# Performance work log

Hardware: AMD Instinct MI355X
Metric: run time of the kernel (lower is better)

The kernel has to match this reference:

```python
import jax, jax.numpy as jnp
import numpy as np

B, L, H = 8, 4096, 1024
S = 32            # sentences (sep tokens) per sample, fixed for stackability
SEP_ID = 102      # BERT [SEP]
NUM_LABELS = 2
LN_EPS = 1e-5


def _make_ids_and_mask():
    rng = np.random.default_rng(0)
    ids = rng.integers(1000, 30000, size=(B, L))
    for i in range(B):
        pos = np.sort(rng.choice(np.arange(1, L), size=S, replace=False))
        ids[i, pos] = SEP_ID
    mask = np.ones((B, L), dtype=np.int32)
    return jnp.asarray(ids, dtype=jnp.int64), jnp.asarray(mask)


def setup_inputs() -> dict:
    key = jax.random.key(0)
    ks = jax.random.split(key, 4)
    input_ids, attention_mask = _make_ids_and_mask()
    std = 0.02
    return {
        "seq": jax.random.normal(ks[0], (B, L, H), dtype=jnp.float32),
        "input_ids": input_ids,
        "attention_mask": attention_mask,
        "W1": jax.random.normal(ks[1], (H, H), dtype=jnp.float32) * std,
        "b1": jnp.zeros((H,), jnp.float32),
        "ln_g": jnp.ones((H,), jnp.float32),
        "ln_b": jnp.zeros((H,), jnp.float32),
        "W2": jax.random.normal(ks[2], (H, NUM_LABELS), dtype=jnp.float32) * std,
        "b2": jnp.zeros((NUM_LABELS,), jnp.float32),
    }


def _segment_means(seq, input_ids, attention_mask):
    # sep positions per sample, fixed count S -> [B, S]
    sep_pos = jax.vmap(
        lambda ids: jnp.nonzero(ids == SEP_ID, size=S, fill_value=L - 1)[0]
    )(input_ids)
    bounds = jnp.concatenate(
        [jnp.zeros((seq.shape[0], 1), sep_pos.dtype), sep_pos], axis=1
    )  # [B, S+1]
    st, ed = bounds[:, :-1], bounds[:, 1:]  # inclusive span [st, ed]

    m = attention_mask.astype(seq.dtype)[..., None]            # [B,L,1]
    # exclusive prefix sums -> sum over [st, ed] = P[ed+1] - P[st]
    P = jnp.pad(jnp.cumsum(seq * m, axis=1), ((0, 0), (1, 0), (0, 0)))   # [B,L+1,H]
    C = jnp.pad(jnp.cumsum(attention_mask.astype(jnp.int32), axis=1), ((0, 0), (1, 0)))

    sums = (jnp.take_along_axis(P, (ed + 1)[..., None], axis=1)
            - jnp.take_along_axis(P, st[..., None], axis=1))   # [B,S,H]
    cnts = (jnp.take_along_axis(C, ed + 1, axis=1)
            - jnp.take_along_axis(C, st, axis=1))              # [B,S]
    cnts = jnp.maximum(cnts, 1).astype(seq.dtype)
    return sums / cnts[..., None]


def reference(seq, input_ids, attention_mask, W1, b1, ln_g, ln_b, W2, b2):
    reps = _segment_means(seq, input_ids, attention_mask)      # [B,S,H]
    h = jnp.einsum("bsh,hk->bsk", reps, W1) + b1
    mu = jnp.mean(h, axis=-1, keepdims=True)
    var = jnp.var(h, axis=-1, keepdims=True)
    h = (h - mu) * jax.lax.rsqrt(var + LN_EPS) * ln_g + ln_b
    h = jax.nn.gelu(h, approximate=False)   # torch nn.GELU default (erf); dropout is eval-mode identity
    return jnp.einsum("bsk,kn->bsn", h, W2) + b2               # [B,S,num_labels]
```

## Files before the change

### kernel.cpp

```cpp
#include <hip/hip_runtime.h>
#include <math.h>

#define BB 8
#define LL 4096
#define HH 1024
#define SS 32
#define SEPID 102
#define NROWS 256
#define TOK 64

__global__ __launch_bounds__(256) void prep_kernel(
    const int* __restrict__ ids, const int* __restrict__ mask,
    float* __restrict__ cnts, unsigned char* __restrict__ segcode) {
  int b = blockIdx.x;
  int tid = threadIdx.x;
  __shared__ int spos_raw[SS];
  __shared__ int spos[SS];
  __shared__ int scnt[SS];
  __shared__ int nsep;
  if (tid == 0) nsep = 0;
  if (tid < SS) { scnt[tid] = 0; spos_raw[tid] = LL - 1; }
  __syncthreads();
  const int* idb = ids + (size_t)b * LL;
  const int* mb  = mask + (size_t)b * LL;
  for (int t = tid; t < LL; t += blockDim.x) {
    if (idb[t] == SEPID) {
      int slot = atomicAdd(&nsep, 1);
      if (slot < SS) spos_raw[slot] = t;
    }
  }
  __syncthreads();
  if (tid < SS) {
    int p = spos_raw[tid];
    int rank = 0;
    for (int j = 0; j < SS; j++) {
      int q = spos_raw[j];
      rank += (q < p) || (q == p && j < tid);
    }
    spos[rank] = p;
  }
  __syncthreads();
  for (int t = tid; t < LL; t += blockDim.x) {
    int r = 0;
#pragma unroll
    for (int j = 0; j < SS; j++) r += (spos[j] < t) ? 1 : 0;
    int issep = (idb[t] == SEPID) ? 1 : 0;
    segcode[(size_t)b * LL + t] = (unsigned char)((r << 1) | issep);
    if (mb[t]) {
      if (issep) {
        atomicAdd(&scnt[r], 1);
        if (r + 1 < SS) atomicAdd(&scnt[r + 1], 1);
      } else if (r < SS) {
        atomicAdd(&scnt[r], 1);
      }
    }
  }
  __syncthreads();
  if (tid < SS) cnts[b * SS + tid] = (float)max(scnt[tid], 1);
}

__device__ __forceinline__ void flush_seg(float* __restrict__ sums, int b,
                                          int seg, int tid, const float4& acc) {
  if (seg >= 0) {
    float* p = sums + ((size_t)(b * SS + seg)) * HH + tid * 4;
    atomicAdd(p + 0, acc.x);
    atomicAdd(p + 1, acc.y);
    atomicAdd(p + 2, acc.z);
    atomicAdd(p + 3, acc.w);
  }
}

__global__ __launch_bounds__(256) void segsum_kernel(
    const float4* __restrict__ seq, const int* __restrict__ mask,
    const unsigned char* __restrict__ segcode, float* __restrict__ sums) {
  const int chunks = LL / TOK;
  int b = blockIdx.x / chunks;
  int c = blockIdx.x % chunks;
  int t0 = c * TOK;
  int tid = threadIdx.x;
  __shared__ int scode[TOK];
  if (tid < TOK) {
    int t = t0 + tid;
    int cd = segcode[(size_t)b * LL + t];
    int m = mask[(size_t)b * LL + t];
    int r = cd >> 1, issep = cd & 1;
    int live = (issep || r < SS) ? 1 : 0;
    scode[tid] = cd | ((m && live) ? 0x100 : 0);
  }
  __syncthreads();
  float4 acc = make_float4(0.f, 0.f, 0.f, 0.f);
  int curseg = -1;
  const float4* rowbase = seq + (size_t)(b * LL + t0) * (HH / 4) + tid;
  for (int i = 0; i < TOK; i++) {
    float4 v = rowbase[(size_t)i * (HH / 4)];
    int cd = scode[i];
    int r = (cd >> 1) & 0x3F;
    int issep = cd & 1;
    float mf = (cd & 0x100) ? 1.f : 0.f;
    v.x *= mf; v.y *= mf; v.z *= mf; v.w *= mf;
    if (issep) {
      if (curseg != r) {
        flush_seg(sums, b, curseg, tid, acc);
        acc = make_float4(0.f, 0.f, 0.f, 0.f);
      }
      acc.x += v.x; acc.y += v.y; acc.z += v.z; acc.w += v.w;
      flush_seg(sums, b, r, tid, acc);
      if (r + 1 < SS) { curseg = r + 1; acc = v; }
      else { curseg = -1; acc = make_float4(0.f, 0.f, 0.f, 0.f); }
    } else {
      int sg = (r < SS) ? r : -1;
      if (sg != curseg) {
        flush_seg(sums, b, curseg, tid, acc);
        curseg = sg;
        acc = make_float4(0.f, 0.f, 0.f, 0.f);
      }
      acc.x += v.x; acc.y += v.y; acc.z += v.z; acc.w += v.w;
    }
  }
  flush_seg(sums, b, curseg, tid, acc);
}

__global__ __launch_bounds__(256) void gemm1_kernel(
    const float* __restrict__ sums, const float* __restrict__ cnts,
    const float* __restrict__ W1, const float* __restrict__ b1,
    float* __restrict__ h1) {
  __shared__ float As[32][33];
  __shared__ float Bs[32][33];
  __shared__ float inv[32];
  int bj = blockIdx.x;
  int bi = blockIdx.y;
  int tid = threadIdx.x;
  int r0 = bi * 32, c0 = bj * 32;
  if (tid < 32) inv[tid] = 1.0f / cnts[r0 + tid];
  __syncthreads();
  int tx = tid & 15, ty = tid >> 4;
  int la_k = tid & 31;
  int la_i = tid >> 5;
  float acc00 = 0.f, acc01 = 0.f, acc10 = 0.f, acc11 = 0.f;
  for (int k0 = 0; k0 < HH; k0 += 32) {
#pragma unroll
    for (int p = 0; p < 4; p++) {
      int i = la_i + p * 8;
      As[i][la_k] = sums[(size_t)(r0 + i) * HH + k0 + la_k] * inv[i];
      Bs[i][la_k] = W1[(size_t)(k0 + i) * HH + c0 + la_k];
    }
    __syncthreads();
#pragma unroll
    for (int kk = 0; kk < 32; kk++) {
      float a0 = As[ty * 2][kk];
      float a1 = As[ty * 2 + 1][kk];
      float b0 = Bs[kk][tx * 2];
      float b1v = Bs[kk][tx * 2 + 1];
      acc00 += a0 * b0; acc01 += a0 * b1v;
      acc10 += a1 * b0; acc11 += a1 * b1v;
    }
    __syncthreads();
  }
  int r = r0 + ty * 2, cc = c0 + tx * 2;
  h1[(size_t)r * HH + cc]           = acc00 + b1[cc];
  h1[(size_t)r * HH + cc + 1]       = acc01 + b1[cc + 1];
  h1[(size_t)(r + 1) * HH + cc]     = acc10 + b1[cc];
  h1[(size_t)(r + 1) * HH + cc + 1] = acc11 + b1[cc + 1];
}

__global__ __launch_bounds__(256) void final_kernel(
    const float* __restrict__ h1, const float* __restrict__ ln_g,
    const float* __restrict__ ln_b, const float* __restrict__ W2,
    const float* __restrict__ b2, float* __restrict__ out) {
  int r = blockIdx.x;
  int tid = threadIdx.x;
  const float4* x4 = (const float4*)(h1 + (size_t)r * HH);
  float4 x = x4[tid];
  float s = x.x + x.y + x.z + x.w;
  float sq = x.x * x.x + x.y * x.y + x.z * x.z + x.w * x.w;
  __shared__ float redA[4], redB[4];
#pragma unroll
  for (int off = 32; off >= 1; off >>= 1) {
    s += __shfl_down(s, off, 64);
    sq += __shfl_down(sq, off, 64);
  }
  int wave = tid >> 6, lane = tid & 63;
  if (lane == 0) { redA[wave] = s; redB[wave] = sq; }
  __syncthreads();
  float ts = redA[0] + redA[1] + redA[2] + redA[3];
  float tq = redB[0] + redB[1] + redB[2] + redB[3];
  float mean = ts * (1.0f / HH);
  float var = tq * (1.0f / HH) - mean * mean;
  float rinv = rsqrtf(var + 1e-5f);
  float4 g4 = ((const float4*)ln_g)[tid];
  float4 bb4 = ((const float4*)ln_b)[tid];
  float xs[4] = {x.x, x.y, x.z, x.w};
  float gs[4] = {g4.x, g4.y, g4.z, g4.w};
  float bs[4] = {bb4.x, bb4.y, bb4.z, bb4.w};
  float o0 = 0.f, o1 = 0.f;
  int h = tid * 4;
#pragma unroll
  for (int j = 0; j < 4; j++) {
    float y = (xs[j] - mean) * rinv * gs[j] + bs[j];
    float gel = 0.5f * y * (1.0f + erff(y * 0.70710678118654752440f));
    o0 += gel * W2[(size_t)(h + j) * 2 + 0];
    o1 += gel * W2[(size_t)(h + j) * 2 + 1];
  }
#pragma unroll
  for (int off = 32; off >= 1; off >>= 1) {
    o0 += __shfl_down(o0, off, 64);
    o1 += __shfl_down(o1, off, 64);
  }
  __syncthreads();
  if (lane == 0) { redA[wave] = o0; redB[wave] = o1; }
  __syncthreads();
  if (tid == 0) {
    float r0 = redA[0] + redA[1] + redA[2] + redA[3] + b2[0];
    float r1 = redB[0] + redB[1] + redB[2] + redB[3] + b2[1];
    out[(size_t)r * 2 + 0] = r0;
    out[(size_t)r * 2 + 1] = r1;
  }
}

extern "C" void kernel_launch(void* const* d_in, const int* in_sizes, int n_in,
                              void* d_out, int out_size, void* d_ws, size_t ws_size,
                              hipStream_t stream) {
  (void)in_sizes; (void)n_in; (void)out_size; (void)ws_size;
  const float* seq  = (const float*)d_in[0];
  const int*   ids  = (const int*)d_in[1];
  const int*   mask = (const int*)d_in[2];
  const float* W1   = (const float*)d_in[3];
  const float* b1   = (const float*)d_in[4];
  const float* ln_g = (const float*)d_in[5];
  const float* ln_b = (const float*)d_in[6];
  const float* W2   = (const float*)d_in[7];
  const float* b2   = (const float*)d_in[8];
  float* out = (float*)d_out;

  char* ws = (char*)d_ws;
  float* sums = (float*)ws;
  float* h1   = (float*)(ws + (1 << 20));
  float* cnts = (float*)(ws + (2 << 20));
  unsigned char* segcode = (unsigned char*)(ws + (2 << 20) + 4096);

  hipMemsetAsync(sums, 0, (size_t)NROWS * HH * sizeof(float), stream);
  prep_kernel<<<BB, 256, 0, stream>>>(ids, mask, cnts, segcode);
  segsum_kernel<<<BB * (LL / TOK), 256, 0, stream>>>(
      (const float4*)seq, mask, segcode, sums);
  dim3 g1(32, 8);
  gemm1_kernel<<<g1, 256, 0, stream>>>(sums, cnts, W1, b1, h1);
  final_kernel<<<NROWS, 256, 0, stream>>>(h1, ln_g, ln_b, W2, b2, out);
}
```

Baseline: 281.2 us.

## Split-K gemm1 with atomics, scan-based counts and binary search in prep

Splits the first GEMM's K dimension four ways across a third grid axis and accumulates partial tiles into a zeroed h1 with float atomics. The b1 bias add moves into the final kernel. The prep kernel now computes segment counts from a block-wide prefix scan of the mask instead of shared atomics, and finds each token's segment index by binary search instead of a 32-way linear scan. The final kernel loads W2 as float4 vectors. This raises GEMM parallelism (256 to 1024 blocks) at the cost of atomic traffic, a larger memset, and non-deterministic summation order.

```diff
diff --git a/kernel.cpp b/kernel.cpp
--- a/kernel.cpp
+++ b/kernel.cpp
@@ -16,14 +16,16 @@
   int tid = threadIdx.x;
   __shared__ int spos_raw[SS];
   __shared__ int spos[SS];
-  __shared__ int scnt[SS];
   __shared__ int nsep;
+  __shared__ int excl_s[257];
+  __shared__ int wtot[4];
   if (tid == 0) nsep = 0;
-  if (tid < SS) { scnt[tid] = 0; spos_raw[tid] = LL - 1; }
+  if (tid < SS) spos_raw[tid] = LL - 1;
   __syncthreads();
   const int* idb = ids + (size_t)b * LL;
   const int* mb  = mask + (size_t)b * LL;
-  for (int t = tid; t < LL; t += blockDim.x) {
+
+  for (int t = tid; t < LL; t += 256) {
     if (idb[t] == SEPID) {
       int slot = atomicAdd(&nsep, 1);
       if (slot < SS) spos_raw[slot] = t;
@@ -39,24 +41,47 @@
     }
     spos[rank] = p;
   }
-  __syncthreads();
-  for (int t = tid; t < LL; t += blockDim.x) {
-    int r = 0;
-#pragma unroll
-    for (int j = 0; j < SS; j++) r += (spos[j] < t) ? 1 : 0;
+
+  int local = 0;
+  int base = tid * 16;
+#pragma unroll
+  for (int i = 0; i < 16; i++) local += mb[base + i];
+  int lane = tid & 63, wave = tid >> 6;
+  int v = local;
+#pragma unroll
+  for (int off = 1; off < 64; off <<= 1) {
+    int n = __shfl_up(v, off, 64);
+    if (lane >= off) v += n;
+  }
+  if (lane == 63) wtot[wave] = v;
+  __syncthreads();
+  int woff = 0;
+  for (int w = 0; w < wave; w++) woff += wtot[w];
+  excl_s[tid] = woff + v - local;
+  if (tid == 0) excl_s[256] = wtot[0] + wtot[1] + wtot[2] + wtot[3];
+  __syncthreads();
+
+  if (tid < SS) {
+    int st = (tid == 0) ? 0 : spos[tid - 1];
+    int ed = spos[tid];
+    int pa = st, pb = ed + 1;
+    int ca = excl_s[pa >> 4];
+    for (int i = pa & ~15; i < pa; i++) ca += mb[i];
+    int cb = excl_s[pb >> 4];
+    for (int i = pb & ~15; i < pb; i++) cb += mb[i];
+    cnts[b * SS + tid] = (float)max(cb - ca, 1);
+  }
+
+  for (int t = tid; t < LL; t += 256) {
+    int lo = 0, hi = SS;
+    while (lo < hi) {
+      int mid = (lo + hi) >> 1;
+      lo = (spos[mid] < t) ? mid + 1 : lo;
+      hi = (spos[mid] < t) ? hi : mid;
+    }
     int issep = (idb[t] == SEPID) ? 1 : 0;
-    segcode[(size_t)b * LL + t] = (unsigned char)((r << 1) | issep);
-    if (mb[t]) {
-      if (issep) {
-        atomicAdd(&scnt[r], 1);
-        if (r + 1 < SS) atomicAdd(&scnt[r + 1], 1);
-      } else if (r < SS) {
-        atomicAdd(&scnt[r], 1);
-      }
-    }
-  }
-  __syncthreads();
-  if (tid < SS) cnts[b * SS + tid] = (float)max(scnt[tid], 1);
+    segcode[(size_t)b * LL + t] = (unsigned char)((lo << 1) | issep);
+  }
 }
 
 __device__ __forceinline__ void flush_seg(float* __restrict__ sums, int b,
@@ -122,22 +147,22 @@
 
 __global__ __launch_bounds__(256) void gemm1_kernel(
     const float* __restrict__ sums, const float* __restrict__ cnts,
-    const float* __restrict__ W1, const float* __restrict__ b1,
-    float* __restrict__ h1) {
+    const float* __restrict__ W1, float* __restrict__ h1) {
   __shared__ float As[32][33];
   __shared__ float Bs[32][33];
   __shared__ float inv[32];
   int bj = blockIdx.x;
   int bi = blockIdx.y;
-  int tid = threadIdx.x;
-  int r0 = bi * 32, c0 = bj * 32;
+  int bz = blockIdx.z;
+  int tid = threadIdx.x;
+  int r0 = bi * 32, c0 = bj * 32, kb = bz * 256;
   if (tid < 32) inv[tid] = 1.0f / cnts[r0 + tid];
   __syncthreads();
   int tx = tid & 15, ty = tid >> 4;
   int la_k = tid & 31;
   int la_i = tid >> 5;
   float acc00 = 0.f, acc01 = 0.f, acc10 = 0.f, acc11 = 0.f;
-  for (int k0 = 0; k0 < HH; k0 += 32) {
+  for (int k0 = kb; k0 < kb + 256; k0 += 32) {
 #pragma unroll
     for (int p = 0; p < 4; p++) {
       int i = la_i + p * 8;
@@ -157,20 +182,22 @@
     __syncthreads();
   }
   int r = r0 + ty * 2, cc = c0 + tx * 2;
-  h1[(size_t)r * HH + cc]           = acc00 + b1[cc];
-  h1[(size_t)r * HH + cc + 1]       = acc01 + b1[cc + 1];
-  h1[(size_t)(r + 1) * HH + cc]     = acc10 + b1[cc];
-  h1[(size_t)(r + 1) * HH + cc + 1] = acc11 + b1[cc + 1];
+  atomicAdd(&h1[(size_t)r * HH + cc], acc00);
+  atomicAdd(&h1[(size_t)r * HH + cc + 1], acc01);
+  atomicAdd(&h1[(size_t)(r + 1) * HH + cc], acc10);
+  atomicAdd(&h1[(size_t)(r + 1) * HH + cc + 1], acc11);
 }
 
 __global__ __launch_bounds__(256) void final_kernel(
-    const float* __restrict__ h1, const float* __restrict__ ln_g,
-    const float* __restrict__ ln_b, const float* __restrict__ W2,
-    const float* __restrict__ b2, float* __restrict__ out) {
+    const float* __restrict__ h1, const float* __restrict__ b1,
+    const float* __restrict__ ln_g, const float* __restrict__ ln_b,
+    const float* __restrict__ W2, const float* __restrict__ b2,
+    float* __restrict__ out) {
   int r = blockIdx.x;
   int tid = threadIdx.x;
-  const float4* x4 = (const float4*)(h1 + (size_t)r * HH);
-  float4 x = x4[tid];
+  float4 x = ((const float4*)(h1 + (size_t)r * HH))[tid];
+  float4 bb1 = ((const float4*)b1)[tid];
+  x.x += bb1.x; x.y += bb1.y; x.z += bb1.z; x.w += bb1.w;
   float s = x.x + x.y + x.z + x.w;
   float sq = x.x * x.x + x.y * x.y + x.z * x.z + x.w * x.w;
   __shared__ float redA[4], redB[4];
@@ -189,17 +216,20 @@
   float rinv = rsqrtf(var + 1e-5f);
   float4 g4 = ((const float4*)ln_g)[tid];
   float4 bb4 = ((const float4*)ln_b)[tid];
+  float4 w20 = ((const float4*)W2)[tid * 2];
+  float4 w21 = ((const float4*)W2)[tid * 2 + 1];
   float xs[4] = {x.x, x.y, x.z, x.w};
   float gs[4] = {g4.x, g4.y, g4.z, g4.w};
   float bs[4] = {bb4.x, bb4.y, bb4.z, bb4.w};
+  float w0[4] = {w20.x, w20.z, w21.x, w21.z};
+  float w1[4] = {w20.y, w20.w, w21.y, w21.w};
   float o0 = 0.f, o1 = 0.f;
-  int h = tid * 4;
 #pragma unroll
   for (int j = 0; j < 4; j++) {
     float y = (xs[j] - mean) * rinv * gs[j] + bs[j];
     float gel = 0.5f * y * (1.0f + erff(y * 0.70710678118654752440f));
-    o0 += gel * W2[(size_t)(h + j) * 2 + 0];
-    o1 += gel * W2[(size_t)(h + j) * 2 + 1];
+    o0 += gel * w0[j];
+    o1 += gel * w1[j];
   }
 #pragma unroll
   for (int off = 32; off >= 1; off >>= 1) {
@@ -210,10 +240,8 @@
   if (lane == 0) { redA[wave] = o0; redB[wave] = o1; }
   __syncthreads();
   if (tid == 0) {
-    float r0 = redA[0] + redA[1] + redA[2] + redA[3] + b2[0];
-    float r1 = redB[0] + redB[1] + redB[2] + redB[3] + b2[1];
-    out[(size_t)r * 2 + 0] = r0;
-    out[(size_t)r * 2 + 1] = r1;
+    out[(size_t)r * 2 + 0] = redA[0] + redA[1] + redA[2] + redA[3] + b2[0];
+    out[(size_t)r * 2 + 1] = redB[0] + redB[1] + redB[2] + redB[3] + b2[1];
   }
 }
 
@@ -238,11 +266,11 @@
   float* cnts = (float*)(ws + (2 << 20));
   unsigned char* segcode = (unsigned char*)(ws + (2 << 20) + 4096);
 
-  hipMemsetAsync(sums, 0, (size_t)NROWS * HH * sizeof(float), stream);
+  hipMemsetAsync(ws, 0, 2u << 20, stream);
   prep_kernel<<<BB, 256, 0, stream>>>(ids, mask, cnts, segcode);
   segsum_kernel<<<BB * (LL / TOK), 256, 0, stream>>>(
       (const float4*)seq, mask, segcode, sums);
-  dim3 g1(32, 8);
-  gemm1_kernel<<<g1, 256, 0, stream>>>(sums, cnts, W1, b1, h1);
-  final_kernel<<<NROWS, 256, 0, stream>>>(h1, ln_g, ln_b, W2, b2, out);
-}
+  dim3 g1(32, 8, 4);
+  gemm1_kernel<<<g1, 256, 0, stream>>>(sums, cnts, W1, h1);
+  final_kernel<<<NROWS, 256, 0, stream>>>(h1, b1, ln_g, ln_b, W2, b2, out);
+}
```

Result: faster. 262.1 us (-6.8%).
